# Kernel tuning notes

Measured on AMD Instinct MI355X. Metric: run time of the kernel, lower is better.

Reference implementation:

```python
import jax, jax.numpy as jnp
import numpy as np

N, E, D, R = 8192, 131072, 128, 32
SIZES = (3, 5, 7)  # per-degree component counts (2l+1)
LN_EPS = 1e-5


def setup_inputs() -> dict:
    key = jax.random.key(0)
    ks = jax.random.split(key, 20)
    rn = lambda k, shape, s=1.0: jax.random.normal(k, shape, jnp.float32) * s
    inp = {
        'X0': rn(ks[0], (N, SIZES[0], D)),
        'X1': rn(ks[1], (N, SIZES[1], D)),
        'X2': rn(ks[2], (N, SIZES[2], D)),
        't_ij': rn(ks[3], (E, D)),
        'r0': rn(ks[4], (E, SIZES[0])),
        'r1': rn(ks[5], (E, SIZES[1])),
        'r2': rn(ks[6], (E, SIZES[2])),
        'edge_index': jax.random.randint(ks[7], (2, E), 0, N, dtype=jnp.int32),
        # params
        'W_vq': rn(ks[8], (D, R), D ** -0.5),
        'W_vk0': rn(ks[9], (D, R), D ** -0.5),
        'W_vk1': rn(ks[10], (D, R), D ** -0.5),
        'W_vk2': rn(ks[11], (D, R), D ** -0.5),
        'ln_g': jnp.ones((R,), jnp.float32),
        'ln_b': jnp.zeros((R,), jnp.float32),
        'W_w': rn(ks[12], (R, D), R ** -0.5),
        'b_w': jnp.zeros((D,), jnp.float32),
        'W_t1': rn(ks[13], (D, D), D ** -0.5),
        'b_t1': jnp.zeros((D,), jnp.float32),
        'W_t2': rn(ks[14], (D, D), D ** -0.5),
        'b_t2': jnp.zeros((D,), jnp.float32),
    }
    return inp


def _vec_rej(x, r):
    # x: [E, L, R], r: [E, L]; dot over component dim (L), keepdim, subtract projection
    r = r[..., None]
    dot = jnp.sum(x * r, axis=1, keepdims=True)  # [E, 1, R]
    return x - dot * r


def reference(X0, X1, X2, t_ij, r0, r1, r2, edge_index,
              W_vq, W_vk0, W_vk1, W_vk2, ln_g, ln_b, W_w, b_w,
              W_t1, b_t1, W_t2, b_t2):
    n_j, n_i = edge_index[0], edge_index[1]
    X_ls = jnp.concatenate([X0, X1, X2], axis=1)                 # [N, 15, D]
    eq_i = jnp.einsum('nld,dr->nlr', X_ls, W_vq)[n_i]            # [E, 15, R]
    ek = jnp.concatenate([
        jnp.einsum('nld,dr->nlr', X0, W_vk0),
        jnp.einsum('nld,dr->nlr', X1, W_vk1),
        jnp.einsum('nld,dr->nlr', X2, W_vk2)], axis=1)
    ek_j = ek[n_j]                                               # [E, 15, R]
    # per-degree vector rejection (vec_rej=True)
    qs, ksl, off = [], [], 0
    for r in (r0, r1, r2):
        s = r.shape[1]
        qs.append(_vec_rej(eq_i[:, off:off + s], r))
        ksl.append(_vec_rej(ek_j[:, off:off + s], -r))
        off += s
    eq_i = jnp.concatenate(qs, axis=1)
    ek_j = jnp.concatenate(ksl, axis=1)
    w_ij = jnp.sum(eq_i * ek_j, axis=1)                          # [E, R]
    # mlp_w = LayerNorm + Linear
    mu = jnp.mean(w_ij, axis=-1, keepdims=True)
    var = jnp.var(w_ij, axis=-1, keepdims=True)
    wn = (w_ij - mu) * jax.lax.rsqrt(var + LN_EPS) * ln_g + ln_b
    dw = wn @ W_w + b_w                                          # [E, D]
    # mlp_t = Linear -> silu -> Linear, then outer activation
    t = jax.nn.silu(t_ij @ W_t1 + b_t1) @ W_t2 + b_t2            # [E, D]
    return dw * jax.nn.silu(t)
```

## Files before the change

kernel.cpp:

```cpp
#include <hip/hip_runtime.h>
#include <hip/hip_bf16.h>

#define N_NODES 8192
#define N_EDGES 131072
#define LN_EPS  1e-5f

typedef __attribute__((ext_vector_type(8))) short bf16x8;
typedef __attribute__((ext_vector_type(4))) float f32x4;

__device__ __forceinline__ float silu_f(float x) {
    return x * __builtin_amdgcn_rcpf(1.0f + __expf(-x));
}

__device__ __forceinline__ unsigned short f2bf(float x) {
    union { float f; unsigned int u; } v; v.f = x;
    unsigned int r = v.u + 0x7FFFu + ((v.u >> 16) & 1u);
    return (unsigned short)(r >> 16);
}
__device__ __forceinline__ float bf2f(unsigned short u) {
    union { float f; unsigned int x; } v; v.x = ((unsigned int)u) << 16;
    return v.f;
}
__device__ __forceinline__ unsigned int pk2(float a, float b) {
    float2 t; t.x = a; t.y = b;
    union { __hip_bfloat162 h; unsigned int u; } v;
    v.h = __float22bfloat162_rn(t);
    return v.u;
}
__device__ __forceinline__ bf16x8 pack8(float4 u, float4 v) {
    union { bf16x8 b; unsigned int w[4]; } o;
    o.w[0] = pk2(u.x, u.y); o.w[1] = pk2(u.z, u.w);
    o.w[2] = pk2(v.x, v.y); o.w[3] = pk2(v.z, v.w);
    return o.b;
}
__device__ __forceinline__ f32x4 mfma16(bf16x8 a, bf16x8 b, f32x4 c) {
    return __builtin_amdgcn_mfma_f32_16x16x32_bf16(a, b, c, 0, 0, 0);
}

__global__ __launch_bounds__(256) void prep_kernel(
    const float* __restrict__ W_w, const float* __restrict__ W_t1,
    const float* __restrict__ W_t2, const float* __restrict__ Wvq,
    const float* __restrict__ Wvk0, const float* __restrict__ Wvk1,
    const float* __restrict__ Wvk2,
    unsigned short* __restrict__ Wtw, unsigned short* __restrict__ Wt1b,
    unsigned short* __restrict__ Wt2b, unsigned short* __restrict__ Wqt,
    unsigned short* __restrict__ Wk0t, unsigned short* __restrict__ Wk1t,
    unsigned short* __restrict__ Wk2t)
{
    int i = blockIdx.x * 256 + threadIdx.x;
    if (i < 16384) {
        int n = i >> 7, k = i & 127;
        Wt1b[i] = f2bf(W_t1[k * 128 + n]);
        Wt2b[i] = f2bf(W_t2[k * 128 + n]);
    }
    if (i < 4096) {
        { int n = i >> 5, k = i & 31; Wtw[i] = f2bf(W_w[k * 128 + n]); }
        int r = i >> 7, d = i & 127;
        Wqt[i]  = f2bf(Wvq [d * 32 + r]);
        Wk0t[i] = f2bf(Wvk0[d * 32 + r]);
        Wk1t[i] = f2bf(Wvk1[d * 32 + r]);
        Wk2t[i] = f2bf(Wvk2[d * 32 + r]);
    }
}

template<int S, int LOFF>
__device__ __forceinline__ void proj_body(
    const float* __restrict__ X, const unsigned short* __restrict__ Wqt,
    const unsigned short* __restrict__ Wkt,
    unsigned short* __restrict__ eq, unsigned short* __restrict__ ek,
    int row0)
{
    const int tid  = threadIdx.x;
    const int lane = tid & 63;
    const int wv   = tid >> 6;
    const int l15  = lane & 15;
    const int lk   = lane >> 4;
    const int xrow = row0 + wv * 16 + l15;

    bf16x8 xf[4];
    #pragma unroll
    for (int kt = 0; kt < 4; ++kt) {
        const float* p = X + (size_t)xrow * 128 + kt * 32 + lk * 8;
        xf[kt] = pack8(*(const float4*)p, *(const float4*)(p + 4));
    }

    f32x4 qa[2], ka[2];
    #pragma unroll
    for (int h = 0; h < 2; ++h) {
        qa[h] = (f32x4){0.f, 0.f, 0.f, 0.f};
        ka[h] = (f32x4){0.f, 0.f, 0.f, 0.f};
    }
    #pragma unroll
    for (int kt = 0; kt < 4; ++kt) {
        #pragma unroll
        for (int h = 0; h < 2; ++h) {
            bf16x8 wq = *(const bf16x8*)&Wqt[(h * 16 + l15) * 128 + kt * 32 + lk * 8];
            bf16x8 wk = *(const bf16x8*)&Wkt[(h * 16 + l15) * 128 + kt * 32 + lk * 8];
            qa[h] = mfma16(wq, xf[kt], qa[h]);
            ka[h] = mfma16(wk, xf[kt], ka[h]);
        }
    }

    const int n = xrow / S;
    const int l = xrow % S + LOFF;
    const size_t base = (size_t)n * 512 + l;
    #pragma unroll
    for (int h = 0; h < 2; ++h) {
        #pragma unroll
        for (int j = 0; j < 4; ++j) {
            const int r = h * 16 + lk * 4 + j;
            eq[base + r * 16] = f2bf(qa[h][j]);
            ek[base + r * 16] = f2bf(ka[h][j]);
        }
    }
}

__global__ __launch_bounds__(256) void proj_kernel(
    const float* __restrict__ X0, const float* __restrict__ X1,
    const float* __restrict__ X2,
    const unsigned short* __restrict__ Wqt,
    const unsigned short* __restrict__ Wk0t,
    const unsigned short* __restrict__ Wk1t,
    const unsigned short* __restrict__ Wk2t,
    unsigned short* __restrict__ eq, unsigned short* __restrict__ ek)
{
    const int b = blockIdx.x;
    if (b < 384)
        proj_body<3, 0>(X0, Wqt, Wk0t, eq, ek, b * 64);
    else if (b < 1024)
        proj_body<5, 3>(X1, Wqt, Wk1t, eq, ek, (b - 384) * 64);
    else
        proj_body<7, 8>(X2, Wqt, Wk2t, eq, ek, (b - 1024) * 64);
}

__device__ __forceinline__ float edge_w(
    bf16x8 q0, bf16x8 q1, bf16x8 k0, bf16x8 k1, const float* rv)
{
    float qv[15], kv[15];
    #pragma unroll
    for (int l = 0; l < 8; ++l) {
        qv[l] = bf2f((unsigned short)q0[l]);
        kv[l] = bf2f((unsigned short)k0[l]);
    }
    #pragma unroll
    for (int l = 8; l < 15; ++l) {
        qv[l] = bf2f((unsigned short)q1[l - 8]);
        kv[l] = bf2f((unsigned short)k1[l - 8]);
    }
    float qk = 0.f;
    #pragma unroll
    for (int l = 0; l < 15; ++l) qk = fmaf(qv[l], kv[l], qk);
    float c0 = 2.f, c1 = 2.f, c2 = 2.f;
    #pragma unroll
    for (int l = 0; l < 3; ++l)  c0 -= rv[l] * rv[l];
    #pragma unroll
    for (int l = 3; l < 8; ++l)  c1 -= rv[l] * rv[l];
    #pragma unroll
    for (int l = 8; l < 15; ++l) c2 -= rv[l] * rv[l];
    float dq0 = 0.f, dk0 = 0.f, dq1 = 0.f, dk1 = 0.f, dq2 = 0.f, dk2 = 0.f;
    #pragma unroll
    for (int l = 0; l < 3; ++l)  { dq0 = fmaf(qv[l], rv[l], dq0); dk0 = fmaf(kv[l], rv[l], dk0); }
    #pragma unroll
    for (int l = 3; l < 8; ++l)  { dq1 = fmaf(qv[l], rv[l], dq1); dk1 = fmaf(kv[l], rv[l], dk1); }
    #pragma unroll
    for (int l = 8; l < 15; ++l) { dq2 = fmaf(qv[l], rv[l], dq2); dk2 = fmaf(kv[l], rv[l], dk2); }
    return qk - dq0 * dk0 * c0 - dq1 * dk1 * c1 - dq2 * dk2 * c2;
}

__global__ __launch_bounds__(256) void wn_kernel(
    const unsigned short* __restrict__ eq, const unsigned short* __restrict__ ek,
    const float* __restrict__ r0, const float* __restrict__ r1,
    const float* __restrict__ r2, const int* __restrict__ eidx,
    const float* __restrict__ ln_g, const float* __restrict__ ln_b,
    unsigned short* __restrict__ wn)
{
    const int tid = threadIdx.x;
    const int r   = tid & 31;
    const int hw  = tid >> 5;
    const int e0  = blockIdx.x * 16 + hw * 2;
    const int e1  = e0 + 1;
    const float g  = ln_g[r];
    const float bb = ln_b[r];

    const int nj0 = eidx[e0], ni0 = eidx[N_EDGES + e0];
    const int nj1 = eidx[e1], ni1 = eidx[N_EDGES + e1];

    const unsigned short* qp0 = eq + (size_t)ni0 * 512 + r * 16;
    const unsigned short* kp0 = ek + (size_t)nj0 * 512 + r * 16;
    const unsigned short* qp1 = eq + (size_t)ni1 * 512 + r * 16;
    const unsigned short* kp1 = ek + (size_t)nj1 * 512 + r * 16;
    bf16x8 qa0 = *(const bf16x8*)qp0, qb0 = *(const bf16x8*)(qp0 + 8);
    bf16x8 ka0 = *(const bf16x8*)kp0, kb0 = *(const bf16x8*)(kp0 + 8);
    bf16x8 qa1 = *(const bf16x8*)qp1, qb1 = *(const bf16x8*)(qp1 + 8);
    bf16x8 ka1 = *(const bf16x8*)kp1, kb1 = *(const bf16x8*)(kp1 + 8);

    float rva[15], rvb[15];
    #pragma unroll
    for (int c = 0; c < 3; ++c) { rva[c]     = r0[e0 * 3 + c]; rvb[c]     = r0[e1 * 3 + c]; }
    #pragma unroll
    for (int c = 0; c < 5; ++c) { rva[3 + c] = r1[e0 * 5 + c]; rvb[3 + c] = r1[e1 * 5 + c]; }
    #pragma unroll
    for (int c = 0; c < 7; ++c) { rva[8 + c] = r2[e0 * 7 + c]; rvb[8 + c] = r2[e1 * 7 + c]; }

    const float w0 = edge_w(qa0, qb0, ka0, kb0, rva);
    const float w1 = edge_w(qa1, qb1, ka1, kb1, rvb);

    float s0 = w0, s20 = w0 * w0, s1 = w1, s21 = w1 * w1;
    #pragma unroll
    for (int off = 1; off < 32; off <<= 1) {
        s0  += __shfl_xor(s0,  off); s20 += __shfl_xor(s20, off);
        s1  += __shfl_xor(s1,  off); s21 += __shfl_xor(s21, off);
    }
    const float mu0   = s0 * (1.f / 32.f);
    const float var0  = s20 * (1.f / 32.f) - mu0 * mu0;
    const float mu1   = s1 * (1.f / 32.f);
    const float var1  = s21 * (1.f / 32.f) - mu1 * mu1;
    wn[(size_t)e0 * 32 + r] = f2bf((w0 - mu0) * rsqrtf(var0 + LN_EPS) * g + bb);
    wn[(size_t)e1 * 32 + r] = f2bf((w1 - mu1) * rsqrtf(var1 + LN_EPS) * g + bb);
}

__global__ __launch_bounds__(256, 2) void edge_kernel(
    const float* __restrict__ t_ij,
    const unsigned short* __restrict__ wn,
    const unsigned short* __restrict__ Wtw, const float* __restrict__ b_w,
    const unsigned short* __restrict__ Wt1, const float* __restrict__ b_t1,
    const unsigned short* __restrict__ Wt2, const float* __restrict__ b_t2,
    float* __restrict__ out)
{
    __shared__ __align__(16) unsigned short Hp[4][64 * 128];

    const int tid  = threadIdx.x;
    const int lane = tid & 63;
    const int wv   = tid >> 6;
    const int l15  = lane & 15;
    const int lk   = lane >> 4;
    const int tile = (blockIdx.x * 4 + wv) * 64;
    char* hp = (char*)&Hp[wv][0];
    const int swz = (l15 & 7) << 4;

    bf16x8 a1[4][4];
    #pragma unroll
    for (int kt = 0; kt < 4; ++kt)
        #pragma unroll
        for (int rt = 0; rt < 4; ++rt) {
            const float* p = t_ij + (size_t)(tile + rt * 16 + l15) * 128
                           + kt * 32 + lk * 8;
            a1[kt][rt] = pack8(*(const float4*)p, *(const float4*)(p + 4));
        }

    bf16x8 wnf[4];
    #pragma unroll
    for (int rt = 0; rt < 4; ++rt)
        wnf[rt] = *(const bf16x8*)&wn[(size_t)(tile + rt * 16 + l15) * 32 + lk * 8];

    bf16x8 w1f[8][4];
    #pragma unroll
    for (int ct = 0; ct < 8; ++ct)
        #pragma unroll
        for (int kt = 0; kt < 4; ++kt)
            w1f[ct][kt] = *(const bf16x8*)&Wt1[(size_t)(ct * 16 + l15) * 128
                                               + kt * 32 + lk * 8];

    #pragma unroll
    for (int ct = 0; ct < 8; ++ct) {
        f32x4 ac[4];
        #pragma unroll
        for (int rt = 0; rt < 4; ++rt) ac[rt] = (f32x4){0.f, 0.f, 0.f, 0.f};
        #pragma unroll
        for (int kt = 0; kt < 4; ++kt)
            #pragma unroll
            for (int rt = 0; rt < 4; ++rt)
                ac[rt] = mfma16(w1f[ct][kt], a1[kt][rt], ac[rt]);

        const float4 bt1 = *(const float4*)&b_t1[ct * 16 + lk * 4];
        #pragma unroll
        for (int rt = 0; rt < 4; ++rt) {
            uint2 hh;
            hh.x = pk2(silu_f(ac[rt][0] + bt1.x), silu_f(ac[rt][1] + bt1.y));
            hh.y = pk2(silu_f(ac[rt][2] + bt1.z), silu_f(ac[rt][3] + bt1.w));
            *(uint2*)(hp + (((rt * 16 + l15) * 256 + ct * 32 + lk * 8) ^ swz)) = hh;
        }
    }

    bf16x8 w2f[8][4];
    #pragma unroll
    for (int ct = 0; ct < 8; ++ct)
        #pragma unroll
        for (int kt = 0; kt < 4; ++kt)
            w2f[ct][kt] = *(const bf16x8*)&Wt2[(size_t)(ct * 16 + l15) * 128
                                               + kt * 32 + lk * 8];

    bf16x8 a2[4][4];
    #pragma unroll
    for (int kt = 0; kt < 4; ++kt)
        #pragma unroll
        for (int rt = 0; rt < 4; ++rt)
            a2[kt][rt] = *(const bf16x8*)(hp +
                (((rt * 16 + l15) * 256 + kt * 64 + lk * 16) ^ swz));

    #pragma unroll
    for (int ct = 0; ct < 8; ++ct) {
        bf16x8 wwf = *(const bf16x8*)&Wtw[(ct * 16 + l15) * 32 + lk * 8];

        f32x4 o[4], d[4];
        #pragma unroll
        for (int rt = 0; rt < 4; ++rt) o[rt] = (f32x4){0.f, 0.f, 0.f, 0.f};
        #pragma unroll
        for (int kt = 0; kt < 4; ++kt)
            #pragma unroll
            for (int rt = 0; rt < 4; ++rt)
                o[rt] = mfma16(w2f[ct][kt], a2[kt][rt], o[rt]);
        #pragma unroll
        for (int rt = 0; rt < 4; ++rt)
            d[rt] = mfma16(wwf, wnf[rt], (f32x4){0.f, 0.f, 0.f, 0.f});

        const float4 bwv = *(const float4*)&b_w[ct * 16 + lk * 4];
        const float4 b2v = *(const float4*)&b_t2[ct * 16 + lk * 4];
        #pragma unroll
        for (int rt = 0; rt < 4; ++rt) {
            float4 s;
            s.x = (d[rt][0] + bwv.x) * silu_f(o[rt][0] + b2v.x);
            s.y = (d[rt][1] + bwv.y) * silu_f(o[rt][1] + b2v.y);
            s.z = (d[rt][2] + bwv.z) * silu_f(o[rt][2] + b2v.z);
            s.w = (d[rt][3] + bwv.w) * silu_f(o[rt][3] + b2v.w);
            *(float4*)&out[(size_t)(tile + rt * 16 + l15) * 128 + ct * 16 + lk * 4] = s;
        }
    }
}

extern "C" void kernel_launch(void* const* d_in, const int* in_sizes, int n_in,
                              void* d_out, int out_size, void* d_ws, size_t ws_size,
                              hipStream_t stream) {
    (void)in_sizes; (void)n_in; (void)out_size; (void)ws_size;
    const float* X0   = (const float*)d_in[0];
    const float* X1   = (const float*)d_in[1];
    const float* X2   = (const float*)d_in[2];
    const float* t_ij = (const float*)d_in[3];
    const float* r0   = (const float*)d_in[4];
    const float* r1   = (const float*)d_in[5];
    const float* r2   = (const float*)d_in[6];
    const int*   eidx = (const int*)d_in[7];
    const float* Wvq  = (const float*)d_in[8];
    const float* Wvk0 = (const float*)d_in[9];
    const float* Wvk1 = (const float*)d_in[10];
    const float* Wvk2 = (const float*)d_in[11];
    const float* ln_g = (const float*)d_in[12];
    const float* ln_b = (const float*)d_in[13];
    const float* W_w  = (const float*)d_in[14];
    const float* b_w  = (const float*)d_in[15];
    const float* W_t1 = (const float*)d_in[16];
    const float* b_t1 = (const float*)d_in[17];
    const float* W_t2 = (const float*)d_in[18];
    const float* b_t2 = (const float*)d_in[19];
    float* out = (float*)d_out;

    unsigned short* eq   = (unsigned short*)d_ws;
    unsigned short* ek   = eq  + (size_t)N_NODES * 512;
    unsigned short* wn   = ek  + (size_t)N_NODES * 512;
    unsigned short* Wtw  = wn  + (size_t)N_EDGES * 32;
    unsigned short* Wt1b = Wtw  + 4096;
    unsigned short* Wt2b = Wt1b + 16384;
    unsigned short* Wqt  = Wt2b + 16384;
    unsigned short* Wk0t = Wqt  + 4096;
    unsigned short* Wk1t = Wk0t + 4096;
    unsigned short* Wk2t = Wk1t + 4096;

    prep_kernel<<<64, 256, 0, stream>>>(W_w, W_t1, W_t2, Wvq, Wvk0, Wvk1, Wvk2,
                                        Wtw, Wt1b, Wt2b, Wqt, Wk0t, Wk1t, Wk2t);
    proj_kernel<<<1920, 256, 0, stream>>>(X0, X1, X2, Wqt, Wk0t, Wk1t, Wk2t,
                                          eq, ek);
    wn_kernel<<<N_EDGES / 16, 256, 0, stream>>>(eq, ek, r0, r1, r2, eidx,
                                                ln_g, ln_b, wn);
    edge_kernel<<<N_EDGES / 256, 256, 0, stream>>>(t_ij, wn, Wtw, b_w,
                                                   Wt1b, b_t1, Wt2b, b_t2, out);
}
```

Measured before the change: 111.4 us.

## Keep MLP hidden activations in registers using K16 MFMA instead of LDS

```diff
diff --git a/kernel.cpp b/kernel.cpp
--- a/kernel.cpp
+++ b/kernel.cpp
@@ -6,6 +6,7 @@
 #define LN_EPS  1e-5f
 
 typedef __attribute__((ext_vector_type(8))) short bf16x8;
+typedef __attribute__((ext_vector_type(4))) short bf16x4;
 typedef __attribute__((ext_vector_type(4))) float f32x4;
 
 __device__ __forceinline__ float silu_f(float x) {
@@ -33,9 +34,26 @@
     o.w[2] = pk2(v.x, v.y); o.w[3] = pk2(v.z, v.w);
     return o.b;
 }
+__device__ __forceinline__ bf16x4 pack4(float a, float b, float c, float d) {
+    union { bf16x4 v; unsigned int u[2]; } o;
+    o.u[0] = pk2(a, b); o.u[1] = pk2(c, d);
+    return o.v;
+}
 __device__ __forceinline__ f32x4 mfma16(bf16x8 a, bf16x8 b, f32x4 c) {
     return __builtin_amdgcn_mfma_f32_16x16x32_bf16(a, b, c, 0, 0, 0);
 }
+#if __has_builtin(__builtin_amdgcn_mfma_f32_16x16x16bf16_1k)
+__device__ __forceinline__ f32x4 mfma_k16(bf16x4 a, bf16x4 b, f32x4 c) {
+    return __builtin_amdgcn_mfma_f32_16x16x16bf16_1k(a, b, c, 0, 0, 0);
+}
+#else
+__device__ __forceinline__ f32x4 mfma_k16(bf16x4 a, bf16x4 b, f32x4 c) {
+    f32x4 d;
+    asm("v_mfma_f32_16x16x16_bf16 %0, %1, %2, %3"
+        : "=v"(d) : "v"(a), "v"(b), "v"(c));
+    return d;
+}
+#endif
 
 __global__ __launch_bounds__(256) void prep_kernel(
     const float* __restrict__ W_w, const float* __restrict__ W_t1,
@@ -219,7 +237,7 @@
     wn[(size_t)e1 * 32 + r] = f2bf((w1 - mu1) * rsqrtf(var1 + LN_EPS) * g + bb);
 }
 
-__global__ __launch_bounds__(256, 2) void edge_kernel(
+__global__ __launch_bounds__(256) void edge_kernel(
     const float* __restrict__ t_ij,
     const unsigned short* __restrict__ wn,
     const unsigned short* __restrict__ Wtw, const float* __restrict__ b_w,
@@ -227,16 +245,12 @@
     const unsigned short* __restrict__ Wt2, const float* __restrict__ b_t2,
     float* __restrict__ out)
 {
-    __shared__ __align__(16) unsigned short Hp[4][64 * 128];
-
     const int tid  = threadIdx.x;
     const int lane = tid & 63;
     const int wv   = tid >> 6;
     const int l15  = lane & 15;
     const int lk   = lane >> 4;
     const int tile = (blockIdx.x * 4 + wv) * 64;
-    char* hp = (char*)&Hp[wv][0];
-    const int swz = (l15 & 7) << 4;
 
     bf16x8 a1[4][4];
     #pragma unroll
@@ -253,16 +267,14 @@
     for (int rt = 0; rt < 4; ++rt)
         wnf[rt] = *(const bf16x8*)&wn[(size_t)(tile + rt * 16 + l15) * 32 + lk * 8];
 
-    bf16x8 w1f[8][4];
-    #pragma unroll
-    for (int ct = 0; ct < 8; ++ct)
+    bf16x4 h[4][8];
+    #pragma unroll
+    for (int ct = 0; ct < 8; ++ct) {
+        bf16x8 w1f[4];
         #pragma unroll
         for (int kt = 0; kt < 4; ++kt)
-            w1f[ct][kt] = *(const bf16x8*)&Wt1[(size_t)(ct * 16 + l15) * 128
-                                               + kt * 32 + lk * 8];
-
-    #pragma unroll
-    for (int ct = 0; ct < 8; ++ct) {
+            w1f[kt] = *(const bf16x8*)&Wt1[(size_t)(ct * 16 + l15) * 128
+                                           + kt * 32 + lk * 8];
         f32x4 ac[4];
         #pragma unroll
         for (int rt = 0; rt < 4; ++rt) ac[rt] = (f32x4){0.f, 0.f, 0.f, 0.f};
@@ -270,60 +282,41 @@
         for (int kt = 0; kt < 4; ++kt)
             #pragma unroll
             for (int rt = 0; rt < 4; ++rt)
-                ac[rt] = mfma16(w1f[ct][kt], a1[kt][rt], ac[rt]);
+                ac[rt] = mfma16(w1f[kt], a1[kt][rt], ac[rt]);
 
         const float4 bt1 = *(const float4*)&b_t1[ct * 16 + lk * 4];
         #pragma unroll
+        for (int rt = 0; rt < 4; ++rt)
+            h[rt][ct] = pack4(silu_f(ac[rt][0] + bt1.x),
+                              silu_f(ac[rt][1] + bt1.y),
+                              silu_f(ac[rt][2] + bt1.z),
+                              silu_f(ac[rt][3] + bt1.w));
+    }
+
+    #pragma unroll
+    for (int ct2 = 0; ct2 < 8; ++ct2) {
+        bf16x4 w2b[8];
+        #pragma unroll
+        for (int ct1 = 0; ct1 < 8; ++ct1)
+            w2b[ct1] = *(const bf16x4*)&Wt2[(size_t)(ct2 * 16 + l15) * 128
+                                            + ct1 * 16 + lk * 4];
+        bf16x8 wwf = *(const bf16x8*)&Wtw[(ct2 * 16 + l15) * 32 + lk * 8];
+        const float bwv = b_w[ct2 * 16 + l15];
+        const float b2v = b_t2[ct2 * 16 + l15];
+
+        #pragma unroll
         for (int rt = 0; rt < 4; ++rt) {
-            uint2 hh;
-            hh.x = pk2(silu_f(ac[rt][0] + bt1.x), silu_f(ac[rt][1] + bt1.y));
-            hh.y = pk2(silu_f(ac[rt][2] + bt1.z), silu_f(ac[rt][3] + bt1.w));
-            *(uint2*)(hp + (((rt * 16 + l15) * 256 + ct * 32 + lk * 8) ^ swz)) = hh;
-        }
-    }
-
-    bf16x8 w2f[8][4];
-    #pragma unroll
-    for (int ct = 0; ct < 8; ++ct)
-        #pragma unroll
-        for (int kt = 0; kt < 4; ++kt)
-            w2f[ct][kt] = *(const bf16x8*)&Wt2[(size_t)(ct * 16 + l15) * 128
-                                               + kt * 32 + lk * 8];
-
-    bf16x8 a2[4][4];
-    #pragma unroll
-    for (int kt = 0; kt < 4; ++kt)
-        #pragma unroll
-        for (int rt = 0; rt < 4; ++rt)
-            a2[kt][rt] = *(const bf16x8*)(hp +
-                (((rt * 16 + l15) * 256 + kt * 64 + lk * 16) ^ swz));
-
-    #pragma unroll
-    for (int ct = 0; ct < 8; ++ct) {
-        bf16x8 wwf = *(const bf16x8*)&Wtw[(ct * 16 + l15) * 32 + lk * 8];
-
-        f32x4 o[4], d[4];
-        #pragma unroll
-        for (int rt = 0; rt < 4; ++rt) o[rt] = (f32x4){0.f, 0.f, 0.f, 0.f};
-        #pragma unroll
-        for (int kt = 0; kt < 4; ++kt)
+            f32x4 o = (f32x4){0.f, 0.f, 0.f, 0.f};
             #pragma unroll
-            for (int rt = 0; rt < 4; ++rt)
-                o[rt] = mfma16(w2f[ct][kt], a2[kt][rt], o[rt]);
-        #pragma unroll
-        for (int rt = 0; rt < 4; ++rt)
-            d[rt] = mfma16(wwf, wnf[rt], (f32x4){0.f, 0.f, 0.f, 0.f});
-
-        const float4 bwv = *(const float4*)&b_w[ct * 16 + lk * 4];
-        const float4 b2v = *(const float4*)&b_t2[ct * 16 + lk * 4];
-        #pragma unroll
-        for (int rt = 0; rt < 4; ++rt) {
-            float4 s;
-            s.x = (d[rt][0] + bwv.x) * silu_f(o[rt][0] + b2v.x);
-            s.y = (d[rt][1] + bwv.y) * silu_f(o[rt][1] + b2v.y);
-            s.z = (d[rt][2] + bwv.z) * silu_f(o[rt][2] + b2v.z);
-            s.w = (d[rt][3] + bwv.w) * silu_f(o[rt][3] + b2v.w);
-            *(float4*)&out[(size_t)(tile + rt * 16 + l15) * 128 + ct * 16 + lk * 4] = s;
+            for (int ct1 = 0; ct1 < 8; ++ct1)
+                o = mfma_k16(h[rt][ct1], w2b[ct1], o);
+            f32x4 d = mfma16(wnf[rt], wwf, (f32x4){0.f, 0.f, 0.f, 0.f});
+
+            float* op = out + (size_t)(tile + rt * 16 + lk * 4) * 128
+                      + ct2 * 16 + l15;
+            #pragma unroll
+            for (int j = 0; j < 4; ++j)
+                op[j * 128] = (d[j] + bwv) * silu_f(o[j] + b2v);
         }
     }
 }
```

New measurement: 115.2 us. +3.5%, slower.
